# Optimization experiments

Hardware: AMD Instinct MI355X
Metric: run time of the kernel (lower is better)

The kernel has to match this reference:

```python
import jax, jax.numpy as jnp
import numpy as np

ALPHA = 0.25   # FOCAL_LOSS_ALPHA
GAMMA = 2.0    # FOCAL_LOSS_GAMMA


def pairwise_iou(anchor, boxes):
    # anchor [A,4], boxes [M,4] -> [A,M]
    area_b = (boxes[:, 2] - boxes[:, 0]) * (boxes[:, 3] - boxes[:, 1])        # [M]
    area_a = (anchor[:, 2] - anchor[:, 0]) * (anchor[:, 3] - anchor[:, 1])    # [A]
    iw = jnp.clip(jnp.minimum(anchor[:, None, 2], boxes[None, :, 2]) -
                  jnp.maximum(anchor[:, None, 0], boxes[None, :, 0]), 0.0)
    ih = jnp.clip(jnp.minimum(anchor[:, None, 3], boxes[None, :, 3]) -
                  jnp.maximum(anchor[:, None, 1], boxes[None, :, 1]), 0.0)
    inter = iw * ih
    ua = jnp.clip(area_a[:, None] + area_b[None, :] - inter, 1e-8)
    return inter / ua


def _per_image(cls_pred, reg_pred, ann, anchor, aw, ah, acx, acy):
    # cls_pred [A,C], reg_pred [A,4], ann [M,5]
    valid = ann[:, 4] != -1.0                              # padding mask
    p = jnp.clip(cls_pred, 1e-4, 1.0 - 1e-4)
    iou = pairwise_iou(anchor, ann[:, :4])                 # [A,M]
    iou = jnp.where(valid[None, :], iou, -1.0)             # invalid GT never matched
    iou_max = iou.max(axis=1)
    iou_arg = iou.argmax(axis=1)
    assigned = ann[iou_arg]                                # [A,5]
    pos = iou_max >= 0.5
    num_pos = pos.sum().astype(p.dtype)
    C = p.shape[1]
    one_hot = jax.nn.one_hot(assigned[:, 4].astype(jnp.int32), C, dtype=p.dtype)
    # targets: 1 for assigned class on positives, 0 elsewhere on positives,
    # 0 everywhere for IoU<0.4, -1 (ignore) in between
    targets = jnp.where(pos[:, None], one_hot,
                        jnp.where((iou_max < 0.4)[:, None], 0.0, -1.0))
    af = jnp.where(targets == 1.0, ALPHA, 1.0 - ALPHA)
    fw = jnp.where(targets == 1.0, 1.0 - p, p)
    fw = af * fw ** GAMMA
    bce = -(targets * jnp.log(p) + (1.0 - targets) * jnp.log(1.0 - p))
    cls_loss = jnp.where(targets != -1.0, fw * bce, 0.0).sum() / jnp.maximum(num_pos, 1.0)
    gw = assigned[:, 2] - assigned[:, 0]
    gh = assigned[:, 3] - assigned[:, 1]
    gcx = assigned[:, 0] + 0.5 * gw
    gcy = assigned[:, 1] + 0.5 * gh
    gw = jnp.maximum(gw, 1.0)
    gh = jnp.maximum(gh, 1.0)
    t = jnp.stack([(gcx - acx) / aw, (gcy - acy) / ah,
                   jnp.log(gw / aw), jnp.log(gh / ah)], axis=1)
    t = t / jnp.array([[0.1, 0.1, 0.2, 0.2]], dtype=p.dtype)
    diff = jnp.abs(t - reg_pred)
    rl = jnp.where(diff <= 1.0 / 9.0, 0.5 * 9.0 * diff ** 2, diff - 0.5 / 9.0)
    reg_loss = jnp.where(num_pos > 0,
                         (rl * pos[:, None]).sum() / jnp.maximum(4.0 * num_pos, 1.0),
                         0.0)
    return cls_loss, reg_loss


def setup_inputs() -> dict:
    key = jax.random.key(0)
    kc, kr, ka1, ka2, kb1, kb2, kl = jax.random.split(key, 7)
    B, A, C, M = 8, 120000, 80, 32
    classifications = jax.random.uniform(kc, (B, A, C), jnp.float32, 0.001, 0.999)
    regressions = jax.random.normal(kr, (B, A, 4), jnp.float32)
    # anchors: valid boxes with x1<x2, y1<y2
    xy1 = jax.random.uniform(ka1, (1, A, 2), jnp.float32, 0.0, 700.0)
    wh = jax.random.uniform(ka2, (1, A, 2), jnp.float32, 8.0, 200.0)
    anchors = jnp.concatenate([xy1, xy1 + wh], axis=-1)
    # annotations: [B,M,5], last 8 slots per image padded with -1
    gxy1 = jax.random.uniform(kb1, (B, M, 2), jnp.float32, 0.0, 600.0)
    gwh = jax.random.uniform(kb2, (B, M, 2), jnp.float32, 16.0, 250.0)
    labels = jax.random.randint(kl, (B, M, 1), 0, C).astype(jnp.float32)
    annotations = jnp.concatenate([gxy1, gxy1 + gwh, labels], axis=-1)
    pad = jnp.arange(M) >= (M - 8)
    annotations = jnp.where(pad[None, :, None], -1.0, annotations)
    return {"classifications": classifications, "regressions": regressions,
            "anchors": anchors, "annotations": annotations}


def reference(classifications, regressions, anchors, annotations):
    anchor = anchors[0]
    aw = anchor[:, 2] - anchor[:, 0]
    ah = anchor[:, 3] - anchor[:, 1]
    acx = anchor[:, 0] + 0.5 * aw
    acy = anchor[:, 1] + 0.5 * ah
    cls_l, reg_l = jax.vmap(_per_image, in_axes=(0, 0, 0, None, None, None, None, None))(
        classifications, regressions, annotations, anchor, aw, ah, acx, acy)
    return cls_l.mean(keepdims=True), reg_l.mean(keepdims=True)
```

## Files before the change

### kernel.cpp

```cpp
#include <hip/hip_runtime.h>
#include <hip/hip_bf16.h>

constexpr int B_   = 8;
constexpr int A_   = 120000;
constexpr int C_   = 80;
constexpr int M_   = 32;
constexpr int APB  = 256;
constexpr int C4   = C_ / 4;

#define F_LN2 0.69314718056f
#define C0_ (0.75f * F_LN2)
#define C1_ (0.25f * F_LN2)


__device__ __forceinline__ float smooth_l1(float d) {
    return (d <= (1.0f / 9.0f)) ? 4.5f * d * d : d - (0.5f / 9.0f);
}

__device__ __forceinline__ float clampp(float x) {
    return fminf(fmaxf(x, 1e-4f), 1.0f - 1e-4f);
}

__device__ __forceinline__ float f_neg(float p) {
    return C0_ * p * p * (-__log2f(1.0f - p));
}
__device__ __forceinline__ float f_pos(float p) {
    const float q = 1.0f - p;
    return C1_ * q * q * (-__log2f(p));
}

__global__ __launch_bounds__(256) void focal_fused(
    const float* __restrict__ cls,
    const float* __restrict__ reg,
    const float* __restrict__ anc,
    const float* __restrict__ ann,
    float* __restrict__ cls_sum,
    float* __restrict__ reg_sum,
    int*   __restrict__ num_pos)
{
    __shared__ float s_ann[M_ * 5];
    __shared__ float s_mask[APB];
    __shared__ float s_red[2];
    __shared__ int   s_np;

    const int b   = blockIdx.y;
    const int a0  = blockIdx.x * APB;
    const int tid = threadIdx.x;
    const int na  = min(APB, A_ - a0);

    if (tid < M_ * 5) s_ann[tid] = ann[b * M_ * 5 + tid];
    if (tid == 0) { s_red[0] = 0.0f; s_red[1] = 0.0f; s_np = 0; }
    __syncthreads();

    float acc  = 0.0f;
    float rsum = 0.0f;
    int   npos = 0;

    if (tid < na) {
        const int a = a0 + tid;
        const float4 ab = reinterpret_cast<const float4*>(anc)[a];
        const float ax1 = ab.x, ay1 = ab.y, ax2 = ab.z, ay2 = ab.w;
        const float area_a = (ax2 - ax1) * (ay2 - ay1);

        float best = -2.0f;
        int   arg  = 0;
        #pragma unroll 8
        for (int m = 0; m < M_; ++m) {
            const float bx1 = s_ann[m * 5 + 0];
            const float by1 = s_ann[m * 5 + 1];
            const float bx2 = s_ann[m * 5 + 2];
            const float by2 = s_ann[m * 5 + 3];
            const float lab = s_ann[m * 5 + 4];
            float iw = fmaxf(fminf(ax2, bx2) - fmaxf(ax1, bx1), 0.0f);
            float ih = fmaxf(fminf(ay2, by2) - fmaxf(ay1, by1), 0.0f);
            const float inter  = iw * ih;
            const float area_b = (bx2 - bx1) * (by2 - by1);
            const float ua = fmaxf(area_a + area_b - inter, 1e-8f);
            float iou = inter / ua;
            if (lab == -1.0f) iou = -1.0f;
            if (iou > best) { best = iou; arg = m; }
        }

        float mask = 1.0f;
        if (best >= 0.5f) {
            const int code = (int)s_ann[arg * 5 + 4];
            const float gx1 = s_ann[arg * 5 + 0];
            const float gy1 = s_ann[arg * 5 + 1];
            const float gx2 = s_ann[arg * 5 + 2];
            const float gy2 = s_ann[arg * 5 + 3];
            float gw = gx2 - gx1, gh = gy2 - gy1;
            const float gcx = gx1 + 0.5f * gw;
            const float gcy = gy1 + 0.5f * gh;
            gw = fmaxf(gw, 1.0f);
            gh = fmaxf(gh, 1.0f);
            const float aw  = ax2 - ax1, ah = ay2 - ay1;
            const float acx = ax1 + 0.5f * aw;
            const float acy = ay1 + 0.5f * ah;
            const float t0 = ((gcx - acx) / aw) * 10.0f;
            const float t1 = ((gcy - acy) / ah) * 10.0f;
            const float t2 = logf(gw / aw) * 5.0f;
            const float t3 = logf(gh / ah) * 5.0f;
            const float4 rp = reinterpret_cast<const float4*>(reg)[(size_t)b * A_ + a];
            rsum = smooth_l1(fabsf(t0 - rp.x))
                 + smooth_l1(fabsf(t1 - rp.y))
                 + smooth_l1(fabsf(t2 - rp.z))
                 + smooth_l1(fabsf(t3 - rp.w));
            npos = 1;
            const float p = clampp(cls[((size_t)b * A_ + a) * C_ + code]);
            acc = f_pos(p) - f_neg(p);
        } else if (best >= 0.4f) {
            mask = 0.0f;
        }
        s_mask[tid] = mask;
    }
    __syncthreads();

    const float4* cp = reinterpret_cast<const float4*>(cls) + ((size_t)b * A_ + a0) * C4;
    const int total = na * C4;
    for (int t = tid; t < total; t += APB) {
        const int la = t / C4;
        const float m = s_mask[la];
        const float4 v = cp[t];
        float s = f_neg(clampp(v.x));
        s += f_neg(clampp(v.y));
        s += f_neg(clampp(v.z));
        s += f_neg(clampp(v.w));
        acc = fmaf(m, s, acc);
    }

    #pragma unroll
    for (int off = 32; off > 0; off >>= 1) {
        acc  += __shfl_down(acc,  off, 64);
        rsum += __shfl_down(rsum, off, 64);
        npos += __shfl_down(npos, off, 64);
    }
    if ((tid & 63) == 0) {
        atomicAdd(&s_red[1], acc);
        atomicAdd(&s_red[0], rsum);
        atomicAdd(&s_np, npos);
    }
    __syncthreads();
    if (tid == 0) {
        atomicAdd(&cls_sum[b], s_red[1]);
        atomicAdd(&reg_sum[b], s_red[0]);
        atomicAdd(&num_pos[b], s_np);
    }
}

__global__ void focal_finalize(const float* __restrict__ cls_sum,
                               const float* __restrict__ reg_sum,
                               const int*   __restrict__ num_pos,
                               float* __restrict__ out)
{
    if (threadIdx.x == 0) {
        float cm = 0.0f, rm = 0.0f;
        for (int b = 0; b < B_; ++b) {
            const float np = (float)num_pos[b];
            cm += cls_sum[b] / fmaxf(np, 1.0f);
            rm += (np > 0.0f) ? reg_sum[b] / fmaxf(4.0f * np, 1.0f) : 0.0f;
        }
        out[0] = cm / (float)B_;
        out[1] = rm / (float)B_;
    }
}

extern "C" void kernel_launch(void* const* d_in, const int* in_sizes, int n_in,
                              void* d_out, int out_size, void* d_ws, size_t ws_size,
                              hipStream_t stream) {
    const float* cls = (const float*)d_in[0];
    const float* reg = (const float*)d_in[1];
    const float* anc = (const float*)d_in[2];
    const float* ann = (const float*)d_in[3];
    float* out = (float*)d_out;

    float* wsf     = (float*)d_ws;
    float* cls_sum = wsf;
    float* reg_sum = wsf + 8;
    int*   np      = (int*)(wsf + 16);

    hipMemsetAsync(d_ws, 0, 24 * sizeof(float), stream);

    dim3 grid((A_ + APB - 1) / APB, B_);
    focal_fused<<<grid, APB, 0, stream>>>(cls, reg, anc, ann, cls_sum, reg_sum, np);
    focal_finalize<<<1, 64, 0, stream>>>(cls_sum, reg_sum, np, out);
}
```

Measured before the change: 457.6 us.

## Replace global atomics with per-block partials and add nontemporal class loads

Each block now writes its partial sums to a dedicated workspace slot instead of using shared and global atomics, and a 1024-thread finalize kernel reduces those partials per image. This drops the memset and the atomic contention on 8 addresses. The class-score stream loop now uses nontemporal vector loads and is unrolled by 4 to raise memory-level parallelism. The cost is an extra pass over about 11K partials per output in the finalize kernel, and num_pos is now accumulated in float.

After: 407.4 us. 11.0% less time.

```diff
diff --git a/kernel.cpp b/kernel.cpp
--- a/kernel.cpp
+++ b/kernel.cpp
@@ -7,10 +7,13 @@
 constexpr int M_   = 32;
 constexpr int APB  = 256;
 constexpr int C4   = C_ / 4;
+constexpr int GX   = (A_ + APB - 1) / APB;
 
 #define F_LN2 0.69314718056f
 #define C0_ (0.75f * F_LN2)
 #define C1_ (0.25f * F_LN2)
+
+typedef float vfloat4 __attribute__((ext_vector_type(4)));
 
 
 __device__ __forceinline__ float smooth_l1(float d) {
@@ -34,14 +37,13 @@
     const float* __restrict__ reg,
     const float* __restrict__ anc,
     const float* __restrict__ ann,
-    float* __restrict__ cls_sum,
-    float* __restrict__ reg_sum,
-    int*   __restrict__ num_pos)
+    float* __restrict__ P_cls,
+    float* __restrict__ P_reg,
+    float* __restrict__ P_np)
 {
     __shared__ float s_ann[M_ * 5];
     __shared__ float s_mask[APB];
-    __shared__ float s_red[2];
-    __shared__ int   s_np;
+    __shared__ float s_red[3][4];
 
     const int b   = blockIdx.y;
     const int a0  = blockIdx.x * APB;
@@ -49,12 +51,11 @@
     const int na  = min(APB, A_ - a0);
 
     if (tid < M_ * 5) s_ann[tid] = ann[b * M_ * 5 + tid];
-    if (tid == 0) { s_red[0] = 0.0f; s_red[1] = 0.0f; s_np = 0; }
     __syncthreads();
 
     float acc  = 0.0f;
     float rsum = 0.0f;
-    int   npos = 0;
+    float npos = 0.0f;
 
     if (tid < na) {
         const int a = a0 + tid;
@@ -105,7 +106,7 @@
                  + smooth_l1(fabsf(t1 - rp.y))
                  + smooth_l1(fabsf(t2 - rp.z))
                  + smooth_l1(fabsf(t3 - rp.w));
-            npos = 1;
+            npos = 1.0f;
             const float p = clampp(cls[((size_t)b * A_ + a) * C_ + code]);
             acc = f_pos(p) - f_neg(p);
         } else if (best >= 0.4f) {
@@ -115,12 +116,13 @@
     }
     __syncthreads();
 
-    const float4* cp = reinterpret_cast<const float4*>(cls) + ((size_t)b * A_ + a0) * C4;
+    const vfloat4* cp = reinterpret_cast<const vfloat4*>(cls) + ((size_t)b * A_ + a0) * C4;
     const int total = na * C4;
+    #pragma unroll 4
     for (int t = tid; t < total; t += APB) {
         const int la = t / C4;
         const float m = s_mask[la];
-        const float4 v = cp[t];
+        const vfloat4 v = __builtin_nontemporal_load(&cp[t]);
         float s = f_neg(clampp(v.x));
         s += f_neg(clampp(v.y));
         s += f_neg(clampp(v.z));
@@ -134,31 +136,58 @@
         rsum += __shfl_down(rsum, off, 64);
         npos += __shfl_down(npos, off, 64);
     }
+    const int wv = tid >> 6;
     if ((tid & 63) == 0) {
-        atomicAdd(&s_red[1], acc);
-        atomicAdd(&s_red[0], rsum);
-        atomicAdd(&s_np, npos);
+        s_red[0][wv] = acc;
+        s_red[1][wv] = rsum;
+        s_red[2][wv] = npos;
     }
     __syncthreads();
     if (tid == 0) {
-        atomicAdd(&cls_sum[b], s_red[1]);
-        atomicAdd(&reg_sum[b], s_red[0]);
-        atomicAdd(&num_pos[b], s_np);
-    }
-}
-
-__global__ void focal_finalize(const float* __restrict__ cls_sum,
-                               const float* __restrict__ reg_sum,
-                               const int*   __restrict__ num_pos,
-                               float* __restrict__ out)
+        const int slot = b * GX + blockIdx.x;
+        P_cls[slot] = s_red[0][0] + s_red[0][1] + s_red[0][2] + s_red[0][3];
+        P_reg[slot] = s_red[1][0] + s_red[1][1] + s_red[1][2] + s_red[1][3];
+        P_np [slot] = s_red[2][0] + s_red[2][1] + s_red[2][2] + s_red[2][3];
+    }
+}
+
+__global__ __launch_bounds__(1024) void focal_finalize(
+    const float* __restrict__ P_cls,
+    const float* __restrict__ P_reg,
+    const float* __restrict__ P_np,
+    float* __restrict__ out)
 {
-    if (threadIdx.x == 0) {
-        float cm = 0.0f, rm = 0.0f;
-        for (int b = 0; b < B_; ++b) {
-            const float np = (float)num_pos[b];
-            cm += cls_sum[b] / fmaxf(np, 1.0f);
-            rm += (np > 0.0f) ? reg_sum[b] / fmaxf(4.0f * np, 1.0f) : 0.0f;
-        }
+    __shared__ float red[3][16];
+    const int tid  = threadIdx.x;
+    const int lane = tid & 63;
+    const int wv   = tid >> 6;
+    float cm = 0.0f, rm = 0.0f;
+
+    for (int b = 0; b < B_; ++b) {
+        float c = 0.0f, r = 0.0f, n = 0.0f;
+        for (int x = tid; x < GX; x += 1024) {
+            c += P_cls[b * GX + x];
+            r += P_reg[b * GX + x];
+            n += P_np [b * GX + x];
+        }
+        #pragma unroll
+        for (int off = 32; off > 0; off >>= 1) {
+            c += __shfl_down(c, off, 64);
+            r += __shfl_down(r, off, 64);
+            n += __shfl_down(n, off, 64);
+        }
+        if (lane == 0) { red[0][wv] = c; red[1][wv] = r; red[2][wv] = n; }
+        __syncthreads();
+        if (tid == 0) {
+            float cs = 0.0f, rs = 0.0f, ns = 0.0f;
+            #pragma unroll
+            for (int w = 0; w < 16; ++w) { cs += red[0][w]; rs += red[1][w]; ns += red[2][w]; }
+            cm += cs / fmaxf(ns, 1.0f);
+            rm += (ns > 0.0f) ? rs / fmaxf(4.0f * ns, 1.0f) : 0.0f;
+        }
+        __syncthreads();
+    }
+    if (tid == 0) {
         out[0] = cm / (float)B_;
         out[1] = rm / (float)B_;
     }
@@ -173,14 +202,12 @@
     const float* ann = (const float*)d_in[3];
     float* out = (float*)d_out;
 
-    float* wsf     = (float*)d_ws;
-    float* cls_sum = wsf;
-    float* reg_sum = wsf + 8;
-    int*   np      = (int*)(wsf + 16);
-
-    hipMemsetAsync(d_ws, 0, 24 * sizeof(float), stream);
-
-    dim3 grid((A_ + APB - 1) / APB, B_);
-    focal_fused<<<grid, APB, 0, stream>>>(cls, reg, anc, ann, cls_sum, reg_sum, np);
-    focal_finalize<<<1, 64, 0, stream>>>(cls_sum, reg_sum, np, out);
-}
+    float* wsf   = (float*)d_ws;
+    float* P_cls = wsf;
+    float* P_reg = wsf + B_ * GX;
+    float* P_np  = wsf + 2 * B_ * GX;
+
+    dim3 grid(GX, B_);
+    focal_fused<<<grid, APB, 0, stream>>>(cls, reg, anc, ann, P_cls, P_reg, P_np);
+    focal_finalize<<<1, 1024, 0, stream>>>(P_cls, P_reg, P_np, out);
+}
```
